# Kernel optimization log

Measured on AMD Instinct MI355X. Metric: run time of the kernel, lower is better.

## Reference

```python
import jax, jax.numpy as jnp
import numpy as np

TAU = 0.5  # config.tau
EPS = 1e-12  # F.normalize eps


def _pair_idx(n_i, hi):
    # all pairs (i, j) with i in [0, n_i), j in (i, hi)
    ii, jj = [], []
    for i in range(n_i):
        js = np.arange(i + 1, hi)
        ii.append(np.full(js.shape, i))
        jj.append(js)
    return np.concatenate(ii), np.concatenate(jj)


def setup_inputs() -> dict:
    key = jax.random.key(0)
    ks = jax.random.split(key, 7)
    B, D, H = 512, 768, 256
    s = 0.02
    return {
        "emb_in": jax.random.normal(ks[0], (B, D), jnp.float32),
        "W1": jax.random.normal(ks[1], (H, 2 * D), jnp.float32) * s,
        "b1": jax.random.normal(ks[2], (H,), jnp.float32) * s,
        "W2": jax.random.normal(ks[3], (H, H), jnp.float32) * s,
        "b2": jax.random.normal(ks[4], (H,), jnp.float32) * s,
        "W3": jax.random.normal(ks[5], (1, H), jnp.float32) * s,
        "b3": jax.random.normal(ks[6], (1,), jnp.float32) * s,
    }


def reference(emb_in, W1, b1, W2, b2, W3, b3):
    B, D = emb_in.shape
    n = B // 4
    m = B // 2

    # L2 normalize rows (torch F.normalize)
    z = emb_in / jnp.maximum(jnp.linalg.norm(emb_in, axis=1, keepdims=True), EPS)
    # cosine similarity matrix [B, B]
    S = z @ z.T

    # ---- ContrastiveLoss (NT-Xent style over first n rows) ----
    logits = S / jnp.asarray(TAU, emb_in.dtype)
    not_diag = 1.0 - jnp.eye(B, dtype=emb_in.dtype)
    denom = jnp.sum(not_diag * jnp.exp(logits), axis=1)  # sum_{k != i} exp(S[i,k]/T)
    log_denom = jnp.log(denom)  # [B]
    ci, cj = _pair_idx(n, n)  # pairs i < j < n
    # loss_ij = -log( exp(S[i,j]/T) / denom_i ) = log_denom[i] - logits[i, j]
    closs_sum = jnp.sum(log_denom[ci] - logits[ci, cj])
    closs = (-2.0 * (n - 1) / n) * closs_sum

    # ---- en_loss: pairwise concat + tiny MLP + BCEWithLogits ----
    ei_np, ej_np = _pair_idx(n, B)  # pairs i in [0,n), j in (i, B)
    ei = jnp.asarray(ei_np)
    ej = jnp.asarray(ej_np)
    labels = (ej_np < m).astype(np.float32)  # first m-(i+1) pairs per i are positives
    labels = jnp.asarray(labels)

    x = jnp.concatenate([z[ei], z[ej]], axis=1)  # [P, 2D]
    h1 = jax.nn.relu(x @ W1.T + b1)              # [P, H]
    h2 = jax.nn.relu(h1 @ W2.T + b2)             # [P, H]
    logit = (h2 @ W3.T + b3)[:, 0]               # [P]

    # BCEWithLogitsLoss (mean), numerically stable form
    bce = jnp.maximum(logit, 0.0) - logit * labels + jnp.log1p(jnp.exp(-jnp.abs(logit)))
    eloss = jnp.mean(bce)

    return closs + eloss
```

## Files before the change

### kernel.cpp

```cpp
#include <hip/hip_runtime.h>
#include <hip/hip_bf16.h>
#include <math.h>

#define B 512
#define D 768
#define H 256
#define NN 128
#define MM 256
#define P_PAIRS 57280
#define NPBLK_P 448

typedef _Float16 f16x8 __attribute__((ext_vector_type(8)));
typedef float f32x4 __attribute__((ext_vector_type(4)));


__global__ __launch_bounds__(256) void k_prep(const float* __restrict__ emb,
                                              const float* __restrict__ W1,
                                              const float* __restrict__ W2,
                                              _Float16* __restrict__ zH,
                                              _Float16* __restrict__ W1H,
                                              _Float16* __restrict__ W2H) {
    __shared__ float invs[8];
    int bx = blockIdx.x;
    int tid = threadIdx.x;
    int w = tid >> 6, lane = tid & 63;

    if (bx < 64) {
        int g8 = bx;
        int grp = g8 >> 1;
        int h = g8 & 1;
        #pragma unroll
        for (int rr = 0; rr < 2; rr++) {
            int r8 = 2 * w + rr;
            const float* rp = emb + (8 * g8 + r8) * D;
            float ss = 0.f;
            #pragma unroll
            for (int it = 0; it < 12; it++) {
                float v = rp[lane + 64 * it];
                ss += v * v;
            }
            #pragma unroll
            for (int m = 1; m <= 32; m <<= 1) ss += __shfl_xor(ss, m);
            if (lane == 0) invs[r8] = 1.0f / fmaxf(sqrtf(ss), 1e-12f);
        }
        __syncthreads();
        #pragma unroll
        for (int it = 0; it < 3; it++) {
            int chunk = it * 256 + tid;
            int s = chunk >> 5;
            int x = chunk & 31;
            int q = x >> 3, r8 = x & 7;
            int r = h * 8 + r8;
            const float* src = emb + (8 * g8 + r8) * D + 32 * s + 8 * q;
            float inv = invs[r8];
            float4 a = *(const float4*)src;
            float4 bb = *(const float4*)(src + 4);
            f16x8 o;
            o[0] = (_Float16)(a.x * inv); o[1] = (_Float16)(a.y * inv);
            o[2] = (_Float16)(a.z * inv); o[3] = (_Float16)(a.w * inv);
            o[4] = (_Float16)(bb.x * inv); o[5] = (_Float16)(bb.y * inv);
            o[6] = (_Float16)(bb.z * inv); o[7] = (_Float16)(bb.w * inv);
            *(f16x8*)(zH + ((grp * 24 + s) * 64 + q * 16 + r) * 8) = o;
        }
    } else if (bx < 128) {
        int g = (bx - 64) >> 1;
        int sh = (bx - 64) & 1;
        #pragma unroll
        for (int it = 0; it < 3; it++) {
            int chunk = it * 256 + tid;
            int s = sh * 12 + (chunk >> 6);
            int lc = chunk & 63;
            int q = lc >> 4, r = lc & 15;
            int n = 16 * g + r;
            const float* src = W1 + (n & 255) * (2 * D) + (n >> 8) * D + 32 * s + 8 * q;
            float4 a = *(const float4*)src;
            float4 bb = *(const float4*)(src + 4);
            f16x8 o;
            o[0] = (_Float16)a.x; o[1] = (_Float16)a.y; o[2] = (_Float16)a.z; o[3] = (_Float16)a.w;
            o[4] = (_Float16)bb.x; o[5] = (_Float16)bb.y; o[6] = (_Float16)bb.z; o[7] = (_Float16)bb.w;
            *(f16x8*)(W1H + ((g * 24 + s) * 64 + lc) * 8) = o;
        }
    } else {
        int g = (bx - 128) >> 1;
        int sh = (bx - 128) & 1;
        int s = sh * 4 + (tid >> 6);
        int lc = tid & 63;
        int q = lc >> 4, r = lc & 15;
        const float* src = W2 + (16 * g + r) * H + 32 * s + 8 * q;
        float4 a = *(const float4*)src;
        float4 bb = *(const float4*)(src + 4);
        f16x8 o;
        o[0] = (_Float16)a.x; o[1] = (_Float16)a.y; o[2] = (_Float16)a.z; o[3] = (_Float16)a.w;
        o[4] = (_Float16)bb.x; o[5] = (_Float16)bb.y; o[6] = (_Float16)bb.z; o[7] = (_Float16)bb.w;
        *(f16x8*)(W2H + ((g * 8 + s) * 64 + lc) * 8) = o;
    }
}

__global__ __launch_bounds__(128) void k_uv(const _Float16* __restrict__ zH,
                                            const _Float16* __restrict__ W1H,
                                            const float* __restrict__ b1,
                                            _Float16* __restrict__ Up,
                                            _Float16* __restrict__ Vv) {
    int w = threadIdx.x >> 6;
    int lane = threadIdx.x & 63;
    int r = lane & 15, q = lane >> 4;
    int gid = blockIdx.x * 2 + w;
    int gm = gid >> 4;
    int gnp = gid & 15;

    f32x4 acc[2] = {};
    #pragma unroll 4
    for (int s = 0; s < 24; s++) {
        f16x8 a = *(const f16x8*)(zH + ((gm * 24 + s) * 64 + lane) * 8);
        #pragma unroll
        for (int nt = 0; nt < 2; nt++) {
            f16x8 bb = *(const f16x8*)(W1H + (((gnp * 2 + nt) * 24 + s) * 64 + lane) * 8);
            acc[nt] = __builtin_amdgcn_mfma_f32_16x16x32_f16(a, bb, acc[nt], 0, 0, 0);
        }
    }
    #pragma unroll
    for (int nt = 0; nt < 2; nt++) {
        int n = (gnp * 2 + nt) * 16 + r;
        float bias = (n < H) ? b1[n] : 0.f;
        #pragma unroll
        for (int rr = 0; rr < 4; rr++) {
            int m = gm * 16 + 4 * q + rr;
            float C = acc[nt][rr] + bias;
            if (n < H) Up[m * H + n] = (_Float16)C;
            else       Vv[m * H + (n - H)] = (_Float16)C;
        }
    }
}

__global__ __launch_bounds__(256, 2) void k_pairs(const _Float16* __restrict__ Up,
                                                  const _Float16* __restrict__ Vv,
                                                  const _Float16* __restrict__ W2H,
                                                  const _Float16* __restrict__ zH,
                                                  const float* __restrict__ b2,
                                                  const float* __restrict__ W3,
                                                  const float* __restrict__ b3,
                                                  float* __restrict__ bcepart,
                                                  float* __restrict__ esp,
                                                  float* __restrict__ slp) {
    int tid = threadIdx.x;
    int w = tid >> 6, lane = tid & 63;
    int r = lane & 15, q = lane >> 4;
    int bx = blockIdx.x;

    if (bx >= NPBLK_P) {
        int t = (bx - NPBLK_P) * 4 + w;
        int gm = t >> 3;
        int slot = t & 7;
        int gn0 = slot * 4;
        f32x4 acc[4] = {};
        #pragma unroll 4
        for (int s = 0; s < 24; s++) {
            f16x8 a = *(const f16x8*)(zH + ((gm * 24 + s) * 64 + lane) * 8);
            #pragma unroll
            for (int nt = 0; nt < 4; nt++) {
                f16x8 bb = *(const f16x8*)(zH + (((gn0 + nt) * 24 + s) * 64 + lane) * 8);
                acc[nt] = __builtin_amdgcn_mfma_f32_16x16x32_f16(a, bb, acc[nt], 0, 0, 0);
            }
        }
        #pragma unroll
        for (int rr = 0; rr < 4; rr++) {
            int irow = gm * 16 + q * 4 + rr;
            float es = 0.f, sl = 0.f;
            #pragma unroll
            for (int nt = 0; nt < 4; nt++) {
                int kcol = (gn0 + nt) * 16 + r;
                float C = acc[nt][rr];
                if (kcol != irow) es += expf(2.f * C);
                if (kcol > irow && kcol < NN) sl += 2.f * C;
            }
            #pragma unroll
            for (int m = 1; m <= 8; m <<= 1) {
                es += __shfl_xor(es, m);
                sl += __shfl_xor(sl, m);
            }
            if (r == 0) {
                esp[slot * NN + irow] = es;
                slp[slot * NN + irow] = sl;
            }
        }
        return;
    }

    __shared__ _Float16 h1[128][264];
    __shared__ float redbuf[4][128];
    __shared__ float red2[2];

    int p0 = bx * 128;

    #pragma unroll
    for (int uu = 0; uu < 2; uu++) {
        int u = uu * 256 + tid;
        int row = u >> 2, cq = u & 3;
        int p = p0 + row;
        if (p >= P_PAIRS) p = P_PAIRS - 1;
        float disc = 1046529.f - 8.f * (float)p;
        int i = (int)((1023.f - sqrtf(disc)) * 0.5f);
        if (i < 0) i = 0;
        if (i > NN - 1) i = NN - 1;
        while (i > 0 && i * (1023 - i) / 2 > p) i--;
        while ((i + 1) * (1022 - i) / 2 <= p) i++;
        int j = i + 1 + (p - i * (1023 - i) / 2);

        const _Float16* up = Up + i * H + 64 * cq;
        const _Float16* vp = Vv + j * H + 64 * cq;
        #pragma unroll
        for (int c8 = 0; c8 < 8; c8++) {
            f16x8 u8 = *(const f16x8*)(up + 8 * c8);
            f16x8 v8 = *(const f16x8*)(vp + 8 * c8);
            f16x8 zero = {};
            f16x8 hv = __builtin_elementwise_max(u8 + v8, zero);
            *(f16x8*)&h1[row][64 * cq + 8 * c8] = hv;
        }
    }
    __syncthreads();

    f32x4 acc[8][4] = {};
    #pragma unroll
    for (int s = 0; s < 8; s++) {
        f16x8 bb[4];
        #pragma unroll
        for (int nt = 0; nt < 4; nt++)
            bb[nt] = *(const f16x8*)(W2H + (((4 * w + nt) * 8 + s) * 64 + lane) * 8);
        #pragma unroll
        for (int mt = 0; mt < 8; mt++) {
            f16x8 a = *(const f16x8*)&h1[16 * mt + r][32 * s + 8 * q];
            #pragma unroll
            for (int nt = 0; nt < 4; nt++)
                acc[mt][nt] = __builtin_amdgcn_mfma_f32_16x16x32_f16(a, bb[nt], acc[mt][nt], 0, 0, 0);
        }
    }

    float b2v[4], w3v[4];
    #pragma unroll
    for (int nt = 0; nt < 4; nt++) {
        int n = 64 * w + 16 * nt + r;
        b2v[nt] = b2[n];
        w3v[nt] = W3[n];
    }
    #pragma unroll
    for (int mt = 0; mt < 8; mt++) {
        float part[4] = {0.f, 0.f, 0.f, 0.f};
        #pragma unroll
        for (int nt = 0; nt < 4; nt++)
            #pragma unroll
            for (int rr = 0; rr < 4; rr++) {
                float h2 = fmaxf(acc[mt][nt][rr] + b2v[nt], 0.f);
                part[rr] += h2 * w3v[nt];
            }
        #pragma unroll
        for (int rr = 0; rr < 4; rr++) {
            float v = part[rr];
            #pragma unroll
            for (int m = 1; m <= 8; m <<= 1) v += __shfl_xor(v, m);
            if (r == 0) redbuf[w][16 * mt + 4 * q + rr] = v;
        }
    }
    __syncthreads();

    if (tid < 128) {
        int p = p0 + tid;
        float lsum = 0.f;
        if (p < P_PAIRS) {
            float disc = 1046529.f - 8.f * (float)p;
            int i = (int)((1023.f - sqrtf(disc)) * 0.5f);
            if (i < 0) i = 0;
            if (i > NN - 1) i = NN - 1;
            while (i > 0 && i * (1023 - i) / 2 > p) i--;
            while ((i + 1) * (1022 - i) / 2 <= p) i++;
            int j = i + 1 + (p - i * (1023 - i) / 2);

            float logit = redbuf[0][tid] + redbuf[1][tid] +
                          redbuf[2][tid] + redbuf[3][tid] + b3[0];
            float label = (j < MM) ? 1.f : 0.f;
            lsum = fmaxf(logit, 0.f) - logit * label + log1pf(expf(-fabsf(logit)));
        }
        #pragma unroll
        for (int off = 32; off > 0; off >>= 1) lsum += __shfl_down(lsum, off);
        if ((tid & 63) == 0) red2[tid >> 6] = lsum;
    }
    __syncthreads();
    if (tid == 0) bcepart[bx] = red2[0] + red2[1];
}

__global__ __launch_bounds__(256) void k_final(const float* __restrict__ esp,
                                               const float* __restrict__ slp,
                                               const float* __restrict__ bcepart,
                                               float* __restrict__ out) {
    __shared__ float red[256];
    int t = threadIdx.x;

    float s = 0.f;
    for (int p = t; p < NPBLK_P; p += 256) s += bcepart[p];
    red[t] = s;
    __syncthreads();
    for (int st = 128; st > 0; st >>= 1) {
        if (t < st) red[t] += red[t + st];
        __syncthreads();
    }
    float bce_total = red[0];
    __syncthreads();

    float v = 0.f;
    if (t < NN) {
        float es = 0.f, sl = 0.f;
        #pragma unroll
        for (int s8 = 0; s8 < 8; s8++) {
            es += esp[s8 * NN + t];
            sl += slp[s8 * NN + t];
        }
        v = (float)(NN - 1 - t) * logf(es) - sl;
    }
    red[t] = v;
    __syncthreads();
    for (int st = 128; st > 0; st >>= 1) {
        if (t < st) red[t] += red[t + st];
        __syncthreads();
    }
    if (t == 0) {
        float closs = (-2.0f * (float)(NN - 1) / (float)NN) * red[0];
        out[0] = closs + bce_total / (float)P_PAIRS;
    }
}

extern "C" void kernel_launch(void* const* d_in, const int* in_sizes, int n_in,
                              void* d_out, int out_size, void* d_ws, size_t ws_size,
                              hipStream_t stream) {
    const float* emb = (const float*)d_in[0];
    const float* W1  = (const float*)d_in[1];
    const float* b1  = (const float*)d_in[2];
    const float* W2  = (const float*)d_in[3];
    const float* b2  = (const float*)d_in[4];
    const float* W3  = (const float*)d_in[5];
    const float* b3  = (const float*)d_in[6];
    float* out = (float*)d_out;

    float* ws = (float*)d_ws;
    float* esp     = ws;
    float* slp     = ws + 1024;
    float* bcepart = ws + 2048;
    _Float16* zH  = (_Float16*)(ws + 3072);
    _Float16* W1H = zH + B * D;
    _Float16* W2H = W1H + 2 * H * D;
    _Float16* Up  = W2H + H * H;
    _Float16* Vv  = Up + B * H;

    k_prep<<<160, 256, 0, stream>>>(emb, W1, W2, zH, W1H, W2H);
    k_uv<<<256, 128, 0, stream>>>(zH, W1H, b1, Up, Vv);
    k_pairs<<<NPBLK_P + 16, 256, 0, stream>>>(Up, Vv, W2H, zH, b2, W3, b3,
                                              bcepart, esp, slp);
    k_final<<<1, 256, 0, stream>>>(esp, slp, bcepart, out);
}
```

Before: 100.6 us.

## Fuse normalization, fp16 conversion, U/V projection and similarity into one kernel

Replaces the prep and U/V kernels with a single fused kernel. It normalizes the A rows on the fly, converts W1 and emb tiles to fp16 in shared memory, and applies the inverse norms after the MFMA. The similarity-row partials also move out of k_pairs into this kernel, which drops one launch and the global zH/W1H round trips. In exchange, each block redundantly reloads and converts W1 and emb tiles through shared memory, and the similarity blocks recompute norms.

```diff
diff --git a/kernel.cpp b/kernel.cpp
--- a/kernel.cpp
+++ b/kernel.cpp
@@ -14,120 +14,167 @@
 typedef float f32x4 __attribute__((ext_vector_type(4)));
 
 
-__global__ __launch_bounds__(256) void k_prep(const float* __restrict__ emb,
-                                              const float* __restrict__ W1,
-                                              const float* __restrict__ W2,
-                                              _Float16* __restrict__ zH,
-                                              _Float16* __restrict__ W1H,
-                                              _Float16* __restrict__ W2H) {
-    __shared__ float invs[8];
+static __device__ __forceinline__ f16x8 cvt8(const float* p) {
+    float4 a = *(const float4*)p;
+    float4 b = *(const float4*)(p + 4);
+    f16x8 o;
+    o[0] = (_Float16)a.x; o[1] = (_Float16)a.y; o[2] = (_Float16)a.z; o[3] = (_Float16)a.w;
+    o[4] = (_Float16)b.x; o[5] = (_Float16)b.y; o[6] = (_Float16)b.z; o[7] = (_Float16)b.w;
+    return o;
+}
+
+__global__ __launch_bounds__(256) void k_fused(const float* __restrict__ emb,
+                                               const float* __restrict__ W1,
+                                               const float* __restrict__ W2,
+                                               const float* __restrict__ b1,
+                                               _Float16* __restrict__ Up,
+                                               _Float16* __restrict__ Vv,
+                                               _Float16* __restrict__ W2H,
+                                               float* __restrict__ esp,
+                                               float* __restrict__ slp) {
+    __shared__ float invA[16];
+    __shared__ _Float16 Afrag[24 * 64 * 8];
+    __shared__ float B32[4][16 * 96];
+    __shared__ float invB[4][64];
+
     int bx = blockIdx.x;
     int tid = threadIdx.x;
     int w = tid >> 6, lane = tid & 63;
-
-    if (bx < 64) {
-        int g8 = bx;
-        int grp = g8 >> 1;
-        int h = g8 & 1;
-        #pragma unroll
-        for (int rr = 0; rr < 2; rr++) {
-            int r8 = 2 * w + rr;
-            const float* rp = emb + (8 * g8 + r8) * D;
+    int r = lane & 15, q = lane >> 4;
+
+    if (bx >= 272) {
+        int rel = bx - 272;
+        #pragma unroll
+        for (int it = 0; it < 4; it++) {
+            int u = rel * 1024 + it * 256 + tid;
+            int g = u >> 9, s = (u >> 6) & 7, lc = u & 63;
+            const float* src = W2 + (16 * g + (lc & 15)) * H + 32 * s + 8 * (lc >> 4);
+            *(f16x8*)(W2H + ((g * 8 + s) * 64 + lc) * 8) = cvt8(src);
+        }
+        return;
+    }
+
+    bool is_sim = (bx >= 256);
+    int gm = is_sim ? ((bx - 256) >> 1) : (bx >> 3);
+
+    {
+        int row = tid >> 4, seg = tid & 15;
+        const float4* rp = (const float4*)(emb + (16 * gm + row) * D) + seg * 12;
+        float ss = 0.f;
+        #pragma unroll
+        for (int j = 0; j < 12; j++) {
+            float4 v = rp[j];
+            ss += v.x * v.x + v.y * v.y + v.z * v.z + v.w * v.w;
+        }
+        #pragma unroll
+        for (int m = 1; m <= 8; m <<= 1) ss += __shfl_xor(ss, m);
+        if (seg == 0) invA[row] = 1.0f / fmaxf(sqrtf(ss), 1e-12f);
+    }
+
+    #pragma unroll
+    for (int it = 0; it < 6; it++) {
+        int u = it * 256 + tid;
+        int s = u >> 6, lc = u & 63;
+        const float* src = emb + (16 * gm + (lc & 15)) * D + 32 * s + 8 * (lc >> 4);
+        *(f16x8*)&Afrag[(s * 64 + lc) * 8] = cvt8(src);
+    }
+    __syncthreads();
+
+    if (!is_sim) {
+        int nb = bx & 7;
+        int n0 = 64 * nb + 16 * w;
+        f32x4 acc = {};
+        float* myB = &B32[w][0];
+
+        for (int c = 0; c < 8; c++) {
+            #pragma unroll
+            for (int it = 0; it < 6; it++) {
+                int f = it * 64 + lane;
+                int rr = f / 24, c4 = f % 24;
+                int n = n0 + rr;
+                const float* src = W1 + (n & 255) * (2 * D) + (n >> 8) * D + 96 * c + 4 * c4;
+                *(float4*)&myB[rr * 96 + 4 * c4] = *(const float4*)src;
+            }
+            #pragma unroll
+            for (int s2 = 0; s2 < 3; s2++) {
+                int s = 3 * c + s2;
+                f16x8 bf = cvt8(&myB[r * 96 + 32 * s2 + 8 * q]);
+                f16x8 a = *(const f16x8*)&Afrag[(s * 64 + lane) * 8];
+                acc = __builtin_amdgcn_mfma_f32_16x16x32_f16(a, bf, acc, 0, 0, 0);
+            }
+        }
+
+        int n = n0 + r;
+        float bias = (n < H) ? b1[n] : 0.f;
+        #pragma unroll
+        for (int rr = 0; rr < 4; rr++) {
+            int m = 16 * gm + 4 * q + rr;
+            float val = acc[rr] * invA[4 * q + rr] + bias;
+            if (n < H) Up[m * H + n] = (_Float16)val;
+            else       Vv[m * H + (n - H)] = (_Float16)val;
+        }
+    } else {
+        int t = (bx - 256) * 4 + w;
+        int slot = t & 7;
+        float* myB = &B32[w][0];
+
+        #pragma unroll
+        for (int p = 0; p < 4; p++) {
+            int rowrel = 16 * p + (lane >> 2);
+            const float* rb = emb + (64 * slot + rowrel) * D;
             float ss = 0.f;
-            #pragma unroll
-            for (int it = 0; it < 12; it++) {
-                float v = rp[lane + 64 * it];
-                ss += v * v;
-            }
-            #pragma unroll
-            for (int m = 1; m <= 32; m <<= 1) ss += __shfl_xor(ss, m);
-            if (lane == 0) invs[r8] = 1.0f / fmaxf(sqrtf(ss), 1e-12f);
-        }
-        __syncthreads();
-        #pragma unroll
-        for (int it = 0; it < 3; it++) {
-            int chunk = it * 256 + tid;
-            int s = chunk >> 5;
-            int x = chunk & 31;
-            int q = x >> 3, r8 = x & 7;
-            int r = h * 8 + r8;
-            const float* src = emb + (8 * g8 + r8) * D + 32 * s + 8 * q;
-            float inv = invs[r8];
-            float4 a = *(const float4*)src;
-            float4 bb = *(const float4*)(src + 4);
-            f16x8 o;
-            o[0] = (_Float16)(a.x * inv); o[1] = (_Float16)(a.y * inv);
-            o[2] = (_Float16)(a.z * inv); o[3] = (_Float16)(a.w * inv);
-            o[4] = (_Float16)(bb.x * inv); o[5] = (_Float16)(bb.y * inv);
-            o[6] = (_Float16)(bb.z * inv); o[7] = (_Float16)(bb.w * inv);
-            *(f16x8*)(zH + ((grp * 24 + s) * 64 + q * 16 + r) * 8) = o;
-        }
-    } else if (bx < 128) {
-        int g = (bx - 64) >> 1;
-        int sh = (bx - 64) & 1;
-        #pragma unroll
-        for (int it = 0; it < 3; it++) {
-            int chunk = it * 256 + tid;
-            int s = sh * 12 + (chunk >> 6);
-            int lc = chunk & 63;
-            int q = lc >> 4, r = lc & 15;
-            int n = 16 * g + r;
-            const float* src = W1 + (n & 255) * (2 * D) + (n >> 8) * D + 32 * s + 8 * q;
-            float4 a = *(const float4*)src;
-            float4 bb = *(const float4*)(src + 4);
-            f16x8 o;
-            o[0] = (_Float16)a.x; o[1] = (_Float16)a.y; o[2] = (_Float16)a.z; o[3] = (_Float16)a.w;
-            o[4] = (_Float16)bb.x; o[5] = (_Float16)bb.y; o[6] = (_Float16)bb.z; o[7] = (_Float16)bb.w;
-            *(f16x8*)(W1H + ((g * 24 + s) * 64 + lc) * 8) = o;
-        }
-    } else {
-        int g = (bx - 128) >> 1;
-        int sh = (bx - 128) & 1;
-        int s = sh * 4 + (tid >> 6);
-        int lc = tid & 63;
-        int q = lc >> 4, r = lc & 15;
-        const float* src = W2 + (16 * g + r) * H + 32 * s + 8 * q;
-        float4 a = *(const float4*)src;
-        float4 bb = *(const float4*)(src + 4);
-        f16x8 o;
-        o[0] = (_Float16)a.x; o[1] = (_Float16)a.y; o[2] = (_Float16)a.z; o[3] = (_Float16)a.w;
-        o[4] = (_Float16)bb.x; o[5] = (_Float16)bb.y; o[6] = (_Float16)bb.z; o[7] = (_Float16)bb.w;
-        *(f16x8*)(W2H + ((g * 8 + s) * 64 + lc) * 8) = o;
-    }
-}
-
-__global__ __launch_bounds__(128) void k_uv(const _Float16* __restrict__ zH,
-                                            const _Float16* __restrict__ W1H,
-                                            const float* __restrict__ b1,
-                                            _Float16* __restrict__ Up,
-                                            _Float16* __restrict__ Vv) {
-    int w = threadIdx.x >> 6;
-    int lane = threadIdx.x & 63;
-    int r = lane & 15, q = lane >> 4;
-    int gid = blockIdx.x * 2 + w;
-    int gm = gid >> 4;
-    int gnp = gid & 15;
-
-    f32x4 acc[2] = {};
-    #pragma unroll 4
-    for (int s = 0; s < 24; s++) {
-        f16x8 a = *(const f16x8*)(zH + ((gm * 24 + s) * 64 + lane) * 8);
-        #pragma unroll
-        for (int nt = 0; nt < 2; nt++) {
-            f16x8 bb = *(const f16x8*)(W1H + (((gnp * 2 + nt) * 24 + s) * 64 + lane) * 8);
-            acc[nt] = __builtin_amdgcn_mfma_f32_16x16x32_f16(a, bb, acc[nt], 0, 0, 0);
-        }
-    }
-    #pragma unroll
-    for (int nt = 0; nt < 2; nt++) {
-        int n = (gnp * 2 + nt) * 16 + r;
-        float bias = (n < H) ? b1[n] : 0.f;
+            #pragma unroll 8
+            for (int it = 0; it < 48; it++) {
+                float4 v = *(const float4*)(rb + 4 * ((lane & 3) + 4 * it));
+                ss += v.x * v.x + v.y * v.y + v.z * v.z + v.w * v.w;
+            }
+            ss += __shfl_xor(ss, 1);
+            ss += __shfl_xor(ss, 2);
+            if ((lane & 3) == 0) invB[w][rowrel] = 1.0f / fmaxf(sqrtf(ss), 1e-12f);
+        }
+
+        f32x4 acc[4] = {};
+        for (int c = 0; c < 8; c++) {
+            #pragma unroll
+            for (int nt = 0; nt < 4; nt++) {
+                #pragma unroll
+                for (int it = 0; it < 6; it++) {
+                    int f = it * 64 + lane;
+                    int rr = f / 24, c4 = f % 24;
+                    const float* src = emb + (64 * slot + 16 * nt + rr) * D + 96 * c + 4 * c4;
+                    *(float4*)&myB[rr * 96 + 4 * c4] = *(const float4*)src;
+                }
+                #pragma unroll
+                for (int s2 = 0; s2 < 3; s2++) {
+                    int s = 3 * c + s2;
+                    f16x8 bf = cvt8(&myB[r * 96 + 32 * s2 + 8 * q]);
+                    f16x8 a = *(const f16x8*)&Afrag[(s * 64 + lane) * 8];
+                    acc[nt] = __builtin_amdgcn_mfma_f32_16x16x32_f16(a, bf, acc[nt], 0, 0, 0);
+                }
+            }
+        }
+
         #pragma unroll
         for (int rr = 0; rr < 4; rr++) {
-            int m = gm * 16 + 4 * q + rr;
-            float C = acc[nt][rr] + bias;
-            if (n < H) Up[m * H + n] = (_Float16)C;
-            else       Vv[m * H + (n - H)] = (_Float16)C;
+            int irow = 16 * gm + 4 * q + rr;
+            float ia = invA[4 * q + rr];
+            float es = 0.f, sl = 0.f;
+            #pragma unroll
+            for (int nt = 0; nt < 4; nt++) {
+                int kcol = 64 * slot + 16 * nt + r;
+                float S = acc[nt][rr] * ia * invB[w][16 * nt + r];
+                if (kcol != irow) es += expf(2.f * S);
+                if (kcol > irow && kcol < NN) sl += 2.f * S;
+            }
+            #pragma unroll
+            for (int m = 1; m <= 8; m <<= 1) {
+                es += __shfl_xor(es, m);
+                sl += __shfl_xor(sl, m);
+            }
+            if (r == 0) {
+                esp[slot * NN + irow] = es;
+                slp[slot * NN + irow] = sl;
+            }
         }
     }
 }
@@ -135,61 +182,18 @@
 __global__ __launch_bounds__(256, 2) void k_pairs(const _Float16* __restrict__ Up,
                                                   const _Float16* __restrict__ Vv,
                                                   const _Float16* __restrict__ W2H,
-                                                  const _Float16* __restrict__ zH,
                                                   const float* __restrict__ b2,
                                                   const float* __restrict__ W3,
                                                   const float* __restrict__ b3,
-                                                  float* __restrict__ bcepart,
-                                                  float* __restrict__ esp,
-                                                  float* __restrict__ slp) {
+                                                  float* __restrict__ bcepart) {
+    __shared__ _Float16 h1[128][264];
+    __shared__ float redbuf[4][128];
+    __shared__ float red2[2];
+
     int tid = threadIdx.x;
     int w = tid >> 6, lane = tid & 63;
     int r = lane & 15, q = lane >> 4;
     int bx = blockIdx.x;
-
-    if (bx >= NPBLK_P) {
-        int t = (bx - NPBLK_P) * 4 + w;
-        int gm = t >> 3;
-        int slot = t & 7;
-        int gn0 = slot * 4;
-        f32x4 acc[4] = {};
-        #pragma unroll 4
-        for (int s = 0; s < 24; s++) {
-            f16x8 a = *(const f16x8*)(zH + ((gm * 24 + s) * 64 + lane) * 8);
-            #pragma unroll
-            for (int nt = 0; nt < 4; nt++) {
-                f16x8 bb = *(const f16x8*)(zH + (((gn0 + nt) * 24 + s) * 64 + lane) * 8);
-                acc[nt] = __builtin_amdgcn_mfma_f32_16x16x32_f16(a, bb, acc[nt], 0, 0, 0);
-            }
-        }
-        #pragma unroll
-        for (int rr = 0; rr < 4; rr++) {
-            int irow = gm * 16 + q * 4 + rr;
-            float es = 0.f, sl = 0.f;
-            #pragma unroll
-            for (int nt = 0; nt < 4; nt++) {
-                int kcol = (gn0 + nt) * 16 + r;
-                float C = acc[nt][rr];
-                if (kcol != irow) es += expf(2.f * C);
-                if (kcol > irow && kcol < NN) sl += 2.f * C;
-            }
-            #pragma unroll
-            for (int m = 1; m <= 8; m <<= 1) {
-                es += __shfl_xor(es, m);
-                sl += __shfl_xor(sl, m);
-            }
-            if (r == 0) {
-                esp[slot * NN + irow] = es;
-                slp[slot * NN + irow] = sl;
-            }
-        }
-        return;
-    }
-
-    __shared__ _Float16 h1[128][264];
-    __shared__ float redbuf[4][128];
-    __shared__ float red2[2];
-
     int p0 = bx * 128;
 
     #pragma unroll
@@ -343,15 +347,11 @@
     float* esp     = ws;
     float* slp     = ws + 1024;
     float* bcepart = ws + 2048;
-    _Float16* zH  = (_Float16*)(ws + 3072);
-    _Float16* W1H = zH + B * D;
-    _Float16* W2H = W1H + 2 * H * D;
+    _Float16* W2H = (_Float16*)(ws + 3072);
     _Float16* Up  = W2H + H * H;
     _Float16* Vv  = Up + B * H;
 
-    k_prep<<<160, 256, 0, stream>>>(emb, W1, W2, zH, W1H, W2H);
-    k_uv<<<256, 128, 0, stream>>>(zH, W1H, b1, Up, Vv);
-    k_pairs<<<NPBLK_P + 16, 256, 0, stream>>>(Up, Vv, W2H, zH, b2, W3, b3,
-                                              bcepart, esp, slp);
+    k_fused<<<280, 256, 0, stream>>>(emb, W1, W2, b1, Up, Vv, W2H, esp, slp);
+    k_pairs<<<NPBLK_P, 256, 0, stream>>>(Up, Vv, W2H, b2, W3, b3, bcepart);
     k_final<<<1, 256, 0, stream>>>(esp, slp, bcepart, out);
 }
```

Result: slower. 148.2 us (+47.3%).
